# Optimization experiments

Measured on AMD Instinct MI355X. Metric: run time of the kernel, lower is better.

Reference implementation:

```python
import jax, jax.numpy as jnp
import numpy as np

N, E, B, EP = 100000, 1600000, 512, 200000
NIN, NEMB, HID, NL = 64, 64, 72, 3
EPS = 1e-5


def setup_inputs() -> dict:
    key = jax.random.key(0)
    ks = jax.random.split(key, 20)
    inp = {
        'x': jax.random.normal(ks[0], (N, NIN), jnp.float32),
        'emb': jax.random.normal(ks[1], (N, NEMB), jnp.float32),
        'assign': jax.random.uniform(ks[2], (N, B), jnp.float32),
        'edge_index': jax.random.randint(ks[3], (2, E), 0, N, jnp.int64),
        'pedge_index': jax.random.randint(ks[4], (2, EP), 0, B, jnp.int64),
        # params (xavier-ish scale)
        'node_w': jax.random.normal(ks[5], (NIN, HID), jnp.float32) / np.sqrt(NIN),
        'node_b': jnp.zeros((HID,), jnp.float32),
        'emb_w': jax.random.normal(ks[6], (NEMB, HID), jnp.float32) / np.sqrt(NEMB),
        'emb_b': jnp.zeros((HID,), jnp.float32),
        'conv_winit': jax.random.normal(ks[7], (NL, HID, HID), jnp.float32) / np.sqrt(HID),
        'conv_wroot': jax.random.normal(ks[8], (NL, HID, HID), jnp.float32) / np.sqrt(HID),
        'conv_bias': jnp.zeros((NL, HID), jnp.float32),
        'bn_gamma': jnp.ones((NL, HID), jnp.float32),
        'bn_beta': jnp.zeros((NL, HID), jnp.float32),
        'mlp_w1': jax.random.normal(ks[9], (12 * HID, HID), jnp.float32) / np.sqrt(12 * HID),
        'mlp_b1': jnp.zeros((HID,), jnp.float32),
        'mlp_w2': jax.random.normal(ks[10], (HID, 1), jnp.float32) / np.sqrt(HID),
        'mlp_b2': jnp.zeros((1,), jnp.float32),
    }
    return inp


def _forward(x, emb, assign, node_w, node_b, emb_w, emb_b, conv_winit,
             conv_wroot, conv_bias, bn_gamma, bn_beta, mlp_w1, mlp_b1,
             mlp_w2, mlp_b2, edge_index, pedge_index):
    n = x.shape[0]
    nb = assign.shape[1]
    row, col = edge_index[0], edge_index[1]
    # gcn_norm without self-loops (ARMAConv): D^{-1/2} A D^{-1/2}
    deg = jax.ops.segment_sum(jnp.ones((row.shape[0],), x.dtype), col, num_segments=n)
    dis = jnp.where(deg > 0, jax.lax.rsqrt(jnp.maximum(deg, 1.0)) * jnp.where(deg > 0, 1.0, 0.0), 0.0)
    dis = jnp.where(deg > 0, deg ** -0.5, 0.0)
    norm = dis[row] * dis[col]

    h = jax.nn.relu(x @ node_w + node_b)  # [N, HID]
    for l in range(NL):
        # ARMAConv K=1, T=1: relu(A_hat (h Wi) + h Wr + b)
        m = norm[:, None] * (h @ conv_winit[l])[row]        # [E, HID]
        agg = jax.ops.segment_sum(m, col, num_segments=n)   # [N, HID]
        h = jax.nn.relu(agg + h @ conv_wroot[l] + conv_bias[l])
        # F.relu applied again in forward (idempotent), then BatchNorm (training stats)
        mu = h.mean(0)
        var = ((h - mu) ** 2).mean(0)
        h = (h - mu) * jax.lax.rsqrt(var + EPS) * bn_gamma[l] + bn_beta[l]

    e = jax.nn.relu(emb @ emb_w + emb_b)
    z = jnp.concatenate([h, e], axis=-1)  # [N, 2*HID]

    batch = jnp.argmax(assign, axis=-1)
    cnt = jax.ops.segment_sum(jnp.ones((n,), z.dtype), batch, num_segments=nb)
    p1 = jax.ops.segment_sum(z, batch, num_segments=nb)
    p2 = jax.ops.segment_max(z, batch, num_segments=nb)
    p3 = p1 / jnp.maximum(cnt, 1.0)[:, None]
    xp = jnp.concatenate([p1, p2, p3], axis=-1)  # [B, 6*HID]

    pair = jnp.concatenate([xp[pedge_index[0]], xp[pedge_index[1]]], axis=1)  # [EP, 12*HID]
    out = jnp.tanh(pair @ mlp_w1 + mlp_b1) @ mlp_w2 + mlp_b2
    return out


def reference(x, emb, assign, edge_index, pedge_index, node_w, node_b, emb_w,
              emb_b, conv_winit, conv_wroot, conv_bias, bn_gamma, bn_beta,
              mlp_w1, mlp_b1, mlp_w2, mlp_b2):
    return _forward(x, emb, assign, node_w, node_b, emb_w, emb_b, conv_winit,
                    conv_wroot, conv_bias, bn_gamma, bn_beta, mlp_w1, mlp_b1,
                    mlp_w2, mlp_b2, edge_index, pedge_index)
```

## Files before the change

### kernel.cpp

```cpp
#include <hip/hip_runtime.h>
#include <hip/hip_bf16.h>

#define HID 72
#define EPSV 1e-5f
#define CAP 64
#define DP 76
#define NSH 32
#define GF 256
#define GA 2048

__device__ __forceinline__ float tanh_fast(float x) {
    float cx = fminf(fmaxf(x, -15.f), 15.f);
    float e = __expf(2.f * cx);
    return __fdividef(e - 1.f, e + 1.f);
}
__device__ __forceinline__ void fma4(float4& a, float w, const float4 v) {
    a.x += w * v.x; a.y += w * v.y; a.z += w * v.z; a.w += w * v.w;
}
__device__ __forceinline__ void add4(float4& a, const float4 v) {
    a.x += v.x; a.y += v.y; a.z += v.z; a.w += v.w;
}
__device__ __forceinline__ float inv_sqrt_deg(int d) {
    return (d > 0) ? rsqrtf((float)d) : 0.f;
}

__global__ __launch_bounds__(256) void k_d1(const float* __restrict__ x, const float* __restrict__ node_w,
                                            const float* __restrict__ node_b,
                                            const float* __restrict__ emb, const float* __restrict__ emb_w,
                                            const float* __restrict__ emb_b,
                                            float* __restrict__ t_buf, float* __restrict__ e_buf,
                                            int* __restrict__ deg, float* __restrict__ shadows,
                                            int* __restrict__ bcnt, int N, int B, int GD) {
    __shared__ float ws[HID][DP];
    int tid = threadIdx.x;
    int bid = blockIdx.x;
    if (bid >= 2 * GD) {
        int j = (bid - 2 * GD) * 256 + tid;
        if (j < N) deg[j] = 0;
        if (j < 3 * NSH * 2 * HID) shadows[j] = 0.f;
        if (j < B) bcnt[j] = 0;
        return;
    }
    const float* xin; const float* W; const float* bias; float* out;
    if (bid < GD) { xin = x;   W = node_w; bias = node_b; out = t_buf; }
    else          { xin = emb; W = emb_w;  bias = emb_b;  out = e_buf; bid -= GD; }
    int n0 = bid * 128;
    for (int i = tid; i < 64 * HID; i += 256) {
        int k = i / HID, f = i % HID;
        ws[f][k] = W[i];
    }
    __syncthreads();
    int tn = tid & 31;
    int tf = (tid >> 5) * 9;
    float acc[4][9];
    #pragma unroll
    for (int j = 0; j < 9; j++) {
        float b = bias[tf + j];
        acc[0][j] = b; acc[1][j] = b; acc[2][j] = b; acc[3][j] = b;
    }
    int g0 = n0 + tn;
    const float4* xp0 = (const float4*)(xin + (size_t)(g0      < N ? g0      : N - 1) * 64);
    const float4* xp1 = (const float4*)(xin + (size_t)(g0 + 32 < N ? g0 + 32 : N - 1) * 64);
    const float4* xp2 = (const float4*)(xin + (size_t)(g0 + 64 < N ? g0 + 64 : N - 1) * 64);
    const float4* xp3 = (const float4*)(xin + (size_t)(g0 + 96 < N ? g0 + 96 : N - 1) * 64);
    #pragma unroll 2
    for (int k4 = 0; k4 < 16; k4++) {
        float4 h0 = xp0[k4];
        float4 h1 = xp1[k4];
        float4 h2 = xp2[k4];
        float4 h3 = xp3[k4];
        int k = k4 * 4;
        #pragma unroll
        for (int j = 0; j < 9; j++) {
            float4 w = *(const float4*)&ws[tf + j][k];
            acc[0][j] += h0.x * w.x + h0.y * w.y + h0.z * w.z + h0.w * w.w;
            acc[1][j] += h1.x * w.x + h1.y * w.y + h1.z * w.z + h1.w * w.w;
            acc[2][j] += h2.x * w.x + h2.y * w.y + h2.z * w.z + h2.w * w.w;
            acc[3][j] += h3.x * w.x + h3.y * w.y + h3.z * w.z + h3.w * w.w;
        }
    }
    #pragma unroll
    for (int i = 0; i < 4; i++) {
        int gn = n0 + tn + 32 * i;
        if (gn >= N) continue;
        float* dst = out + (size_t)gn * HID + tf;
        #pragma unroll
        for (int j = 0; j < 9; j++) dst[j] = fmaxf(acc[i][j], 0.f);
    }
}

__global__ __launch_bounds__(256) void k_front2(const int* __restrict__ row, const int* __restrict__ col,
                                                int* __restrict__ deg, int* __restrict__ csr_r, int E,
                                                const float* __restrict__ t_buf,
                                                const float* __restrict__ wi0, const float* __restrict__ wr0,
                                                const float* __restrict__ cb0,
                                                float* __restrict__ hw, float* __restrict__ t2,
                                                const float* __restrict__ assign, int* __restrict__ batchv,
                                                int* __restrict__ bcnt, int N, int B, int GC) {
    __shared__ float ws[HID][DP];
    int tid = threadIdx.x;
    int bid = blockIdx.x;

    if (bid < GF) {
        int stride = GF * 256 * 8;
        for (int base = (bid * 256 + tid) * 8; base < E; base += stride) {
            #pragma unroll
            for (int h = 0; h < 2; h++) {
                int eb = base + h * 4;
                if (eb + 3 < E) {
                    int4 cc = *(const int4*)(col + eb);
                    int4 rr = *(const int4*)(row + eb);
                    int p0 = atomicAdd(&deg[cc.x], 1);
                    int p1 = atomicAdd(&deg[cc.y], 1);
                    int p2 = atomicAdd(&deg[cc.z], 1);
                    int p3 = atomicAdd(&deg[cc.w], 1);
                    if (p0 < CAP) csr_r[(size_t)cc.x * CAP + p0] = rr.x;
                    if (p1 < CAP) csr_r[(size_t)cc.y * CAP + p1] = rr.y;
                    if (p2 < CAP) csr_r[(size_t)cc.z * CAP + p2] = rr.z;
                    if (p3 < CAP) csr_r[(size_t)cc.w * CAP + p3] = rr.w;
                } else if (eb < E) {
                    int lim = (eb + 4 < E) ? eb + 4 : E;
                    for (int e = eb; e < lim; e++) {
                        int c = col[e];
                        int pos = atomicAdd(&deg[c], 1);
                        if (pos < CAP) csr_r[(size_t)c * CAP + pos] = row[e];
                    }
                }
            }
        }
        return;
    }
    bid -= GF;
    if (bid < 2 * GC) {
        const float* W; const float* bias; float* out;
        if (bid < GC) { W = wi0; bias = nullptr; out = hw; }
        else          { W = wr0; bias = cb0;     out = t2; bid -= GC; }
        int n0 = bid * 128;
        for (int i = tid; i < HID * HID; i += 256) {
            int k = i / HID, f = i % HID;
            ws[f][k] = W[i];
        }
        __syncthreads();
        int tn = tid & 31;
        int tf = (tid >> 5) * 9;
        float acc[4][9];
        #pragma unroll
        for (int j = 0; j < 9; j++) {
            float b = bias ? bias[tf + j] : 0.f;
            acc[0][j] = b; acc[1][j] = b; acc[2][j] = b; acc[3][j] = b;
        }
        int g0 = n0 + tn;
        const float* r0 = t_buf + (size_t)(g0      < N ? g0      : N - 1) * HID;
        const float* r1 = t_buf + (size_t)(g0 + 32 < N ? g0 + 32 : N - 1) * HID;
        const float* r2 = t_buf + (size_t)(g0 + 64 < N ? g0 + 64 : N - 1) * HID;
        const float* r3 = t_buf + (size_t)(g0 + 96 < N ? g0 + 96 : N - 1) * HID;
        #pragma unroll 2
        for (int k4 = 0; k4 < HID / 4; k4++) {
            int k = k4 * 4;
            float4 h0 = *(const float4*)(r0 + k);
            float4 h1 = *(const float4*)(r1 + k);
            float4 h2 = *(const float4*)(r2 + k);
            float4 h3 = *(const float4*)(r3 + k);
            #pragma unroll
            for (int j = 0; j < 9; j++) {
                float4 w = *(const float4*)&ws[tf + j][k];
                acc[0][j] += h0.x * w.x + h0.y * w.y + h0.z * w.z + h0.w * w.w;
                acc[1][j] += h1.x * w.x + h1.y * w.y + h1.z * w.z + h1.w * w.w;
                acc[2][j] += h2.x * w.x + h2.y * w.y + h2.z * w.z + h2.w * w.w;
                acc[3][j] += h3.x * w.x + h3.y * w.y + h3.z * w.z + h3.w * w.w;
            }
        }
        #pragma unroll
        for (int i = 0; i < 4; i++) {
            int gn = n0 + tn + 32 * i;
            if (gn >= N) continue;
            float* dst = out + (size_t)gn * HID + tf;
            #pragma unroll
            for (int j = 0; j < 9; j++) dst[j] = acc[i][j];
        }
        return;
    }
    bid -= 2 * GC;
    int wib = tid >> 6;
    int lane = tid & 63;
    int nq = B / 4;
    for (int n = bid * 4 + wib; n < N; n += GA * 4) {
        const float4* rp4 = (const float4*)(assign + (size_t)n * B);
        float best = -INFINITY;
        int bidx = 0x7fffffff;
        for (int q = lane; q < nq; q += 64) {
            float4 v = rp4[q];
            int j = q * 4;
            if (v.x > best) { best = v.x; bidx = j; }
            if (v.y > best) { best = v.y; bidx = j + 1; }
            if (v.z > best) { best = v.z; bidx = j + 2; }
            if (v.w > best) { best = v.w; bidx = j + 3; }
        }
        #pragma unroll
        for (int off = 32; off > 0; off >>= 1) {
            float ov = __shfl_down(best, off);
            int oi = __shfl_down(bidx, off);
            if (ov > best || (ov == best && oi < bidx)) { best = ov; bidx = oi; }
        }
        if (lane == 0) {
            batchv[n] = bidx;
            atomicAdd(&bcnt[bidx], 1);
        }
    }
}

template <int SCALED>
__global__ __launch_bounds__(256) void k_gather9(const float* __restrict__ hw, const int* __restrict__ deg,
                                                 const int* __restrict__ csr_r, const float* __restrict__ t2,
                                                 float* __restrict__ t, int N, float* __restrict__ shadow,
                                                 int scanB, const int* __restrict__ bcnt,
                                                 int* __restrict__ boffs, int* __restrict__ bcur) {
    if (scanB && blockIdx.x == gridDim.x - 1) {
        int lane = threadIdx.x;
        if (lane < 64) {
            int c[8];
            int tot = 0;
            int base = lane * 8;
            #pragma unroll
            for (int j = 0; j < 8; j++) {
                int idx = base + j;
                c[j] = (idx < scanB) ? bcnt[idx] : 0;
                tot += c[j];
            }
            int v = tot;
            #pragma unroll
            for (int off = 1; off < 64; off <<= 1) {
                int u = __shfl_up(v, off);
                if (lane >= off) v += u;
            }
            int run = v - tot;
            #pragma unroll
            for (int j = 0; j < 8; j++) {
                int idx = base + j;
                if (idx < scanB) {
                    boffs[idx] = run;
                    bcur[idx] = run;
                    run += c[j];
                }
            }
        }
        return;
    }
    __shared__ float s1[HID], s2[HID];
    int tx = threadIdx.x;
    if (tx < HID) { s1[tx] = 0.f; s2[tx] = 0.f; }
    __syncthreads();
    int tid = blockIdx.x * blockDim.x + tx;
    int n = tid / 9;
    int s = tid - n * 9;
    if (n < N) {
        const float4* t2row = (const float4*)(t2 + (size_t)n * HID) + s * 2;
        float4 a0 = t2row[0], a1 = t2row[1];
        float4 b0 = make_float4(0.f, 0.f, 0.f, 0.f), b1 = b0;
        int dn = deg[n];
        int d = (dn > CAP) ? CAP : dn;
        float disc = inv_sqrt_deg(dn);
        const int* crow = csr_r + (size_t)n * CAP;
        const float4* hb = (const float4*)hw + s * 2;
        for (int j0 = 0; j0 < d; j0 += 4) {
            int4 rr = *(const int4*)(crow + j0);
            int rem = d - j0;
            {
                const float4* hp = hb + (size_t)rr.x * 18;
                if (SCALED) { add4(b0, hp[0]); add4(b1, hp[1]); }
                else { float w = inv_sqrt_deg(deg[rr.x]); fma4(b0, w, hp[0]); fma4(b1, w, hp[1]); }
            }
            if (rem > 1) {
                const float4* hp = hb + (size_t)rr.y * 18;
                if (SCALED) { add4(b0, hp[0]); add4(b1, hp[1]); }
                else { float w = inv_sqrt_deg(deg[rr.y]); fma4(b0, w, hp[0]); fma4(b1, w, hp[1]); }
            }
            if (rem > 2) {
                const float4* hp = hb + (size_t)rr.z * 18;
                if (SCALED) { add4(b0, hp[0]); add4(b1, hp[1]); }
                else { float w = inv_sqrt_deg(deg[rr.z]); fma4(b0, w, hp[0]); fma4(b1, w, hp[1]); }
            }
            if (rem > 3) {
                const float4* hp = hb + (size_t)rr.w * 18;
                if (SCALED) { add4(b0, hp[0]); add4(b1, hp[1]); }
                else { float w = inv_sqrt_deg(deg[rr.w]); fma4(b0, w, hp[0]); fma4(b1, w, hp[1]); }
            }
        }
        fma4(a0, disc, b0);
        fma4(a1, disc, b1);
        a0 = make_float4(fmaxf(a0.x, 0.f), fmaxf(a0.y, 0.f), fmaxf(a0.z, 0.f), fmaxf(a0.w, 0.f));
        a1 = make_float4(fmaxf(a1.x, 0.f), fmaxf(a1.y, 0.f), fmaxf(a1.z, 0.f), fmaxf(a1.w, 0.f));
        float4* trow = (float4*)(t + (size_t)n * HID) + s * 2;
        trow[0] = a0;
        trow[1] = a1;
        int f0 = s * 8;
        atomicAdd(&s1[f0 + 0], a0.x); atomicAdd(&s2[f0 + 0], a0.x * a0.x);
        atomicAdd(&s1[f0 + 1], a0.y); atomicAdd(&s2[f0 + 1], a0.y * a0.y);
        atomicAdd(&s1[f0 + 2], a0.z); atomicAdd(&s2[f0 + 2], a0.z * a0.z);
        atomicAdd(&s1[f0 + 3], a0.w); atomicAdd(&s2[f0 + 3], a0.w * a0.w);
        atomicAdd(&s1[f0 + 4], a1.x); atomicAdd(&s2[f0 + 4], a1.x * a1.x);
        atomicAdd(&s1[f0 + 5], a1.y); atomicAdd(&s2[f0 + 5], a1.y * a1.y);
        atomicAdd(&s1[f0 + 6], a1.z); atomicAdd(&s2[f0 + 6], a1.z * a1.z);
        atomicAdd(&s1[f0 + 7], a1.w); atomicAdd(&s2[f0 + 7], a1.w * a1.w);
    }
    __syncthreads();
    if (tx < HID) {
        float* shrow = shadow + (size_t)(blockIdx.x & (NSH - 1)) * (2 * HID);
        atomicAdd(&shrow[tx], s1[tx]);
        atomicAdd(&shrow[HID + tx], s2[tx]);
    }
}

#define CP 76
__global__ __launch_bounds__(256) void k_conv_t(const float* __restrict__ t, const float* __restrict__ shadow,
                                                const float* __restrict__ gamma, const float* __restrict__ beta,
                                                const float* __restrict__ wi, const float* __restrict__ wr,
                                                const float* __restrict__ cb, float* __restrict__ hw,
                                                float* __restrict__ t2, const int* __restrict__ deg,
                                                int N, float invN, int gcBlocks,
                                                const int* __restrict__ batchv, int* __restrict__ bcur,
                                                int* __restrict__ nlist) {
    __shared__ float hs[64][CP];
    __shared__ float ws[2 * HID][CP];
    __shared__ float bns[2 * HID];
    int tid = threadIdx.x;
    if ((int)blockIdx.x >= gcBlocks) {
        int n = ((int)blockIdx.x - gcBlocks) * 256 + tid;
        if (n < N) {
            int b = batchv[n];
            int pos = atomicAdd(&bcur[b], 1);
            nlist[pos] = n;
        }
        return;
    }
    if (tid < 2 * HID) {
        float ssum = 0.f;
        #pragma unroll
        for (int c = 0; c < NSH; c++) ssum += shadow[c * 2 * HID + tid];
        bns[tid] = ssum;
    }
    for (int i = tid; i < HID * 2 * HID; i += 256) {
        int k = i / (2 * HID), f = i % (2 * HID);
        ws[f][k] = (f < HID) ? wi[k * HID + f] : wr[k * HID + (f - HID)];
    }
    __syncthreads();
    int n0 = blockIdx.x * 64;
    for (int i = tid; i < 64 * HID; i += 256) {
        int n = i / HID, f = i % HID;
        int gn = n0 + n;
        float v = (gn < N) ? t[(size_t)gn * HID + f] : 0.f;
        float mu = bns[f] * invN;
        float var = bns[HID + f] * invN - mu * mu;
        v = (v - mu) * rsqrtf(var + EPSV) * gamma[f] + beta[f];
        hs[n][f] = v;
    }
    __syncthreads();
    int tn = tid & 15;
    int tf = (tid >> 4) * 9;
    float acc[4][9];
    #pragma unroll
    for (int j = 0; j < 9; j++) {
        float b = (tf >= HID) ? cb[tf - HID + j] : 0.f;
        acc[0][j] = b; acc[1][j] = b; acc[2][j] = b; acc[3][j] = b;
    }
    #pragma unroll 2
    for (int k4 = 0; k4 < HID / 4; k4++) {
        int k = k4 * 4;
        float4 h0 = *(const float4*)&hs[tn][k];
        float4 h1 = *(const float4*)&hs[tn + 16][k];
        float4 h2 = *(const float4*)&hs[tn + 32][k];
        float4 h3 = *(const float4*)&hs[tn + 48][k];
        #pragma unroll
        for (int j = 0; j < 9; j++) {
            float4 w = *(const float4*)&ws[tf + j][k];
            acc[0][j] += h0.x * w.x + h0.y * w.y + h0.z * w.z + h0.w * w.w;
            acc[1][j] += h1.x * w.x + h1.y * w.y + h1.z * w.z + h1.w * w.w;
            acc[2][j] += h2.x * w.x + h2.y * w.y + h2.z * w.z + h2.w * w.w;
            acc[3][j] += h3.x * w.x + h3.y * w.y + h3.z * w.z + h3.w * w.w;
        }
    }
    #pragma unroll
    for (int i = 0; i < 4; i++) {
        int gn = n0 + tn + 16 * i;
        if (gn >= N) continue;
        if (tf < HID) {
            float dsc = inv_sqrt_deg(deg[gn]);
            float* dst = hw + (size_t)gn * HID + tf;
            #pragma unroll
            for (int j = 0; j < 9; j++) dst[j] = acc[i][j] * dsc;
        } else {
            float* dst = t2 + (size_t)gn * HID + (tf - HID);
            #pragma unroll
            for (int j = 0; j < 9; j++) dst[j] = acc[i][j];
        }
    }
}

__global__ __launch_bounds__(576) void k_poolB(const float* __restrict__ t2, const float* __restrict__ ebuf,
                                               const float* __restrict__ shadow2, const float* __restrict__ g2,
                                               const float* __restrict__ bt2, const int* __restrict__ boffs,
                                               const int* __restrict__ bcnt, const int* __restrict__ nlist,
                                               float* __restrict__ xp, float invN) {
    __shared__ float ls[4][2 * HID], lm[4][2 * HID];
    int b = blockIdx.x;
    int tid = threadIdx.x;
    int f = tid % (2 * HID);
    int ch = tid / (2 * HID);
    bool isH = f < HID;
    float a = 1.f, sh = 0.f;
    const float* src;
    if (isH) {
        float s1v = 0.f, s2v = 0.f;
        #pragma unroll
        for (int c = 0; c < NSH; c++) {
            s1v += shadow2[c * 2 * HID + f];
            s2v += shadow2[c * 2 * HID + HID + f];
        }
        float mu = s1v * invN;
        float var = s2v * invN - mu * mu;
        float inv = rsqrtf(var + EPSV);
        a = inv * g2[f];
        sh = bt2[f] - mu * a;
        src = t2 + f;
    } else {
        src = ebuf + (f - HID);
    }
    int s = boffs[b];
    int c = bcnt[b];
    int e = s + c;
    float sum = 0.f, mx = -INFINITY;
    for (int i = s + ch; i < e; i += 4) {
        float v = src[(size_t)nlist[i] * HID] * a + sh;
        sum += v;
        mx = fmaxf(mx, v);
    }
    ls[ch][f] = sum;
    lm[ch][f] = mx;
    __syncthreads();
    if (ch == 0) {
        float stot = ls[0][f] + ls[1][f] + ls[2][f] + ls[3][f];
        float mtot = fmaxf(fmaxf(lm[0][f], lm[1][f]), fmaxf(lm[2][f], lm[3][f]));
        float* xr = xp + (size_t)b * (6 * HID);
        xr[f] = stot;
        xr[2 * HID + f] = mtot;
        xr[4 * HID + f] = stot / fmaxf((float)c, 1.f);
    }
}

__global__ __launch_bounds__(192) void k_uv(const float* __restrict__ xp, const float* __restrict__ w1,
                                            const float* __restrict__ b1, float* __restrict__ U,
                                            float* __restrict__ V) {
    int b = blockIdx.x;
    int t = threadIdx.x;
    if (t >= 2 * HID) return;
    int half = t / HID;
    int f = t % HID;
    const float* xr = xp + (size_t)b * (6 * HID);
    const float* wb = w1 + (size_t)half * (6 * HID) * HID + f;
    float acc = (half == 0) ? b1[f] : 0.f;
    #pragma unroll 4
    for (int k = 0; k < 6 * HID; k++) acc += xr[k] * wb[(size_t)k * HID];
    if (half == 0) U[(size_t)b * HID + f] = acc;
    else           V[(size_t)b * HID + f] = acc;
}

__global__ __launch_bounds__(256) void k_edge(const int* __restrict__ pe, const float* __restrict__ U,
                                              const float* __restrict__ V, const float* __restrict__ w2,
                                              const float* __restrict__ b2, float* __restrict__ out, int EP) {
    int ep = blockIdx.x * blockDim.x + threadIdx.x;
    if (ep >= EP) return;
    int a = pe[ep];
    int b = pe[EP + ep];
    const float4* up = (const float4*)(U + (size_t)a * HID);
    const float4* vp = (const float4*)(V + (size_t)b * HID);
    float s = 0.f;
    #pragma unroll
    for (int q = 0; q < HID / 4; q++) {
        float4 u = up[q];
        float4 v = vp[q];
        s += tanh_fast(u.x + v.x) * w2[q * 4 + 0];
        s += tanh_fast(u.y + v.y) * w2[q * 4 + 1];
        s += tanh_fast(u.z + v.z) * w2[q * 4 + 2];
        s += tanh_fast(u.w + v.w) * w2[q * 4 + 3];
    }
    out[ep] = s + b2[0];
}

extern "C" void kernel_launch(void* const* d_in, const int* in_sizes, int n_in,
                              void* d_out, int out_size, void* d_ws, size_t ws_size,
                              hipStream_t stream) {
    const float* x       = (const float*)d_in[0];
    const float* emb     = (const float*)d_in[1];
    const float* assign  = (const float*)d_in[2];
    const int*   ei      = (const int*)d_in[3];
    const int*   pe      = (const int*)d_in[4];
    const float* node_w  = (const float*)d_in[5];
    const float* node_b  = (const float*)d_in[6];
    const float* emb_w   = (const float*)d_in[7];
    const float* emb_b   = (const float*)d_in[8];
    const float* conv_wi = (const float*)d_in[9];
    const float* conv_wr = (const float*)d_in[10];
    const float* conv_b  = (const float*)d_in[11];
    const float* bn_g    = (const float*)d_in[12];
    const float* bn_b    = (const float*)d_in[13];
    const float* w1      = (const float*)d_in[14];
    const float* b1      = (const float*)d_in[15];
    const float* w2      = (const float*)d_in[16];
    const float* b2      = (const float*)d_in[17];

    int N = in_sizes[0] / 64;
    int B = in_sizes[2] / N;
    int E = in_sizes[3] / 2;
    int EP = in_sizes[4] / 2;
    float invN = 1.0f / (float)N;

    char* wp = (char*)d_ws;
    auto alloc = [&](size_t nbytes) -> void* {
        void* p = (void*)wp;
        wp += (nbytes + 255) & ~(size_t)255;
        return p;
    };
    float* t_buf  = (float*)alloc((size_t)N * HID * 4);
    float* t2     = (float*)alloc((size_t)N * HID * 4);
    float* hw     = (float*)alloc((size_t)N * HID * 4);
    float* e_buf  = (float*)alloc((size_t)N * HID * 4);
    int*   csr_r  = (int*)alloc((size_t)N * CAP * 4);
    int*   deg    = (int*)alloc((size_t)N * 4);
    int*   batchv = (int*)alloc((size_t)N * 4);
    int*   nlist  = (int*)alloc((size_t)N * 4);
    float* shadows= (float*)alloc((size_t)3 * NSH * 2 * HID * 4);
    int*   bcnt   = (int*)alloc((size_t)B * 4);
    int*   boffs  = (int*)alloc((size_t)B * 4);
    int*   bcur   = (int*)alloc((size_t)B * 4);
    float* xp     = (float*)alloc((size_t)B * 6 * HID * 4);
    float* Ub     = (float*)alloc((size_t)B * HID * 4);
    float* Vb     = (float*)alloc((size_t)B * HID * 4);

    const int* row = ei;
    const int* col = ei + E;

    int GD   = (N + 127) / 128;
    int GC64 = (N + 63) / 64;
    int GZ   = (N + 255) / 256;
    int GG   = (9 * N + 255) / 256;
    size_t shl = (size_t)NSH * 2 * HID;

    k_d1<<<2 * GD + GZ, 256, 0, stream>>>(x, node_w, node_b, emb, emb_w, emb_b,
                                          t_buf, e_buf, deg, shadows, bcnt, N, B, GD);

    k_front2<<<GF + 2 * GD + GA, 256, 0, stream>>>(row, col, deg, csr_r, E,
                                                   t_buf, conv_wi, conv_wr, conv_b, hw, t2,
                                                   assign, batchv, bcnt, N, B, GD);

    k_gather9<0><<<GG + 1, 256, 0, stream>>>(hw, deg, csr_r, t2, t_buf, N, shadows,
                                             B, bcnt, boffs, bcur);

    k_conv_t<<<GC64 + GZ, 256, 0, stream>>>(t_buf, shadows, bn_g, bn_b,
                                            conv_wi + (size_t)HID * HID, conv_wr + (size_t)HID * HID,
                                            conv_b + HID, hw, t2, deg, N, invN, GC64,
                                            batchv, bcur, nlist);
    k_gather9<1><<<GG, 256, 0, stream>>>(hw, deg, csr_r, t2, t_buf, N, shadows + shl,
                                         0, nullptr, nullptr, nullptr);

    k_conv_t<<<GC64, 256, 0, stream>>>(t_buf, shadows + shl, bn_g + HID, bn_b + HID,
                                       conv_wi + (size_t)2 * HID * HID, conv_wr + (size_t)2 * HID * HID,
                                       conv_b + 2 * HID, hw, t2, deg, N, invN, GC64,
                                       nullptr, nullptr, nullptr);
    k_gather9<1><<<GG, 256, 0, stream>>>(hw, deg, csr_r, t2, t_buf, N, shadows + 2 * shl,
                                         0, nullptr, nullptr, nullptr);

    k_poolB<<<B, 576, 0, stream>>>(t_buf, e_buf, shadows + 2 * shl,
                                   bn_g + 2 * HID, bn_b + 2 * HID,
                                   boffs, bcnt, nlist, xp, invN);
    k_uv<<<B, 192, 0, stream>>>(xp, w1, b1, Ub, Vb);
    k_edge<<<(EP + 255) / 256, 256, 0, stream>>>(pe, Ub, Vb, w2, b2, (float*)d_out, EP);
}
```

Measured before the change: 1.316 ms.

## Split gather into 18 lanes per node, separate BN stats kernel, split conv by weight

```diff
diff --git a/kernel.cpp b/kernel.cpp
--- a/kernel.cpp
+++ b/kernel.cpp
@@ -5,7 +5,6 @@
 #define EPSV 1e-5f
 #define CAP 64
 #define DP 76
-#define NSH 32
 #define GF 256
 #define GA 2048
 
@@ -29,7 +28,7 @@
                                             const float* __restrict__ emb, const float* __restrict__ emb_w,
                                             const float* __restrict__ emb_b,
                                             float* __restrict__ t_buf, float* __restrict__ e_buf,
-                                            int* __restrict__ deg, float* __restrict__ shadows,
+                                            int* __restrict__ deg, float* __restrict__ stats,
                                             int* __restrict__ bcnt, int N, int B, int GD) {
     __shared__ float ws[HID][DP];
     int tid = threadIdx.x;
@@ -37,7 +36,7 @@
     if (bid >= 2 * GD) {
         int j = (bid - 2 * GD) * 256 + tid;
         if (j < N) deg[j] = 0;
-        if (j < 3 * NSH * 2 * HID) shadows[j] = 0.f;
+        if (j < 3 * 2 * HID) stats[j] = 0.f;
         if (j < B) bcnt[j] = 0;
         return;
     }
@@ -210,11 +209,11 @@
 }
 
 template <int SCALED>
-__global__ __launch_bounds__(256) void k_gather9(const float* __restrict__ hw, const int* __restrict__ deg,
-                                                 const int* __restrict__ csr_r, const float* __restrict__ t2,
-                                                 float* __restrict__ t, int N, float* __restrict__ shadow,
-                                                 int scanB, const int* __restrict__ bcnt,
-                                                 int* __restrict__ boffs, int* __restrict__ bcur) {
+__global__ __launch_bounds__(256) void k_gather18(const float* __restrict__ hw, const int* __restrict__ deg,
+                                                  const int* __restrict__ csr_r, const float* __restrict__ t2,
+                                                  float* __restrict__ t, int N,
+                                                  int scanB, const int* __restrict__ bcnt,
+                                                  int* __restrict__ boffs, int* __restrict__ bcur) {
     if (scanB && blockIdx.x == gridDim.x - 1) {
         int lane = threadIdx.x;
         if (lane < 64) {
@@ -246,86 +245,86 @@
         }
         return;
     }
+    int tid = blockIdx.x * blockDim.x + threadIdx.x;
+    int n = tid / 18;
+    int s = tid - n * 18;
+    if (n >= N) return;
+    float4 a0 = *((const float4*)(t2 + (size_t)n * HID) + s);
+    float4 b0 = make_float4(0.f, 0.f, 0.f, 0.f);
+    int dn = deg[n];
+    int d = (dn > CAP) ? CAP : dn;
+    float disc = inv_sqrt_deg(dn);
+    const int* crow = csr_r + (size_t)n * CAP;
+    const float4* hb = (const float4*)hw + s;
+    for (int j0 = 0; j0 < d; j0 += 4) {
+        int4 rr = *(const int4*)(crow + j0);
+        int rem = d - j0;
+        {
+            float4 hv = hb[(size_t)rr.x * 18];
+            if (SCALED) add4(b0, hv); else fma4(b0, inv_sqrt_deg(deg[rr.x]), hv);
+        }
+        if (rem > 1) {
+            float4 hv = hb[(size_t)rr.y * 18];
+            if (SCALED) add4(b0, hv); else fma4(b0, inv_sqrt_deg(deg[rr.y]), hv);
+        }
+        if (rem > 2) {
+            float4 hv = hb[(size_t)rr.z * 18];
+            if (SCALED) add4(b0, hv); else fma4(b0, inv_sqrt_deg(deg[rr.z]), hv);
+        }
+        if (rem > 3) {
+            float4 hv = hb[(size_t)rr.w * 18];
+            if (SCALED) add4(b0, hv); else fma4(b0, inv_sqrt_deg(deg[rr.w]), hv);
+        }
+    }
+    fma4(a0, disc, b0);
+    *((float4*)(t + (size_t)n * HID) + s) =
+        make_float4(fmaxf(a0.x, 0.f), fmaxf(a0.y, 0.f), fmaxf(a0.z, 0.f), fmaxf(a0.w, 0.f));
+}
+
+__global__ __launch_bounds__(256) void k_stats(const float* __restrict__ t, float* __restrict__ st, int total4) {
     __shared__ float s1[HID], s2[HID];
     int tx = threadIdx.x;
-    if (tx < HID) { s1[tx] = 0.f; s2[tx] = 0.f; }
+    if (tx < HID) s1[tx] = 0.f;
+    else if (tx < 2 * HID) s2[tx - HID] = 0.f;
     __syncthreads();
-    int tid = blockIdx.x * blockDim.x + tx;
-    int n = tid / 9;
-    int s = tid - n * 9;
-    if (n < N) {
-        const float4* t2row = (const float4*)(t2 + (size_t)n * HID) + s * 2;
-        float4 a0 = t2row[0], a1 = t2row[1];
-        float4 b0 = make_float4(0.f, 0.f, 0.f, 0.f), b1 = b0;
-        int dn = deg[n];
-        int d = (dn > CAP) ? CAP : dn;
-        float disc = inv_sqrt_deg(dn);
-        const int* crow = csr_r + (size_t)n * CAP;
-        const float4* hb = (const float4*)hw + s * 2;
-        for (int j0 = 0; j0 < d; j0 += 4) {
-            int4 rr = *(const int4*)(crow + j0);
-            int rem = d - j0;
-            {
-                const float4* hp = hb + (size_t)rr.x * 18;
-                if (SCALED) { add4(b0, hp[0]); add4(b1, hp[1]); }
-                else { float w = inv_sqrt_deg(deg[rr.x]); fma4(b0, w, hp[0]); fma4(b1, w, hp[1]); }
-            }
-            if (rem > 1) {
-                const float4* hp = hb + (size_t)rr.y * 18;
-                if (SCALED) { add4(b0, hp[0]); add4(b1, hp[1]); }
-                else { float w = inv_sqrt_deg(deg[rr.y]); fma4(b0, w, hp[0]); fma4(b1, w, hp[1]); }
-            }
-            if (rem > 2) {
-                const float4* hp = hb + (size_t)rr.z * 18;
-                if (SCALED) { add4(b0, hp[0]); add4(b1, hp[1]); }
-                else { float w = inv_sqrt_deg(deg[rr.z]); fma4(b0, w, hp[0]); fma4(b1, w, hp[1]); }
-            }
-            if (rem > 3) {
-                const float4* hp = hb + (size_t)rr.w * 18;
-                if (SCALED) { add4(b0, hp[0]); add4(b1, hp[1]); }
-                else { float w = inv_sqrt_deg(deg[rr.w]); fma4(b0, w, hp[0]); fma4(b1, w, hp[1]); }
-            }
-        }
-        fma4(a0, disc, b0);
-        fma4(a1, disc, b1);
-        a0 = make_float4(fmaxf(a0.x, 0.f), fmaxf(a0.y, 0.f), fmaxf(a0.z, 0.f), fmaxf(a0.w, 0.f));
-        a1 = make_float4(fmaxf(a1.x, 0.f), fmaxf(a1.y, 0.f), fmaxf(a1.z, 0.f), fmaxf(a1.w, 0.f));
-        float4* trow = (float4*)(t + (size_t)n * HID) + s * 2;
-        trow[0] = a0;
-        trow[1] = a1;
-        int f0 = s * 8;
-        atomicAdd(&s1[f0 + 0], a0.x); atomicAdd(&s2[f0 + 0], a0.x * a0.x);
-        atomicAdd(&s1[f0 + 1], a0.y); atomicAdd(&s2[f0 + 1], a0.y * a0.y);
-        atomicAdd(&s1[f0 + 2], a0.z); atomicAdd(&s2[f0 + 2], a0.z * a0.z);
-        atomicAdd(&s1[f0 + 3], a0.w); atomicAdd(&s2[f0 + 3], a0.w * a0.w);
-        atomicAdd(&s1[f0 + 4], a1.x); atomicAdd(&s2[f0 + 4], a1.x * a1.x);
-        atomicAdd(&s1[f0 + 5], a1.y); atomicAdd(&s2[f0 + 5], a1.y * a1.y);
-        atomicAdd(&s1[f0 + 6], a1.z); atomicAdd(&s2[f0 + 6], a1.z * a1.z);
-        atomicAdd(&s1[f0 + 7], a1.w); atomicAdd(&s2[f0 + 7], a1.w * a1.w);
-    }
+    int stride = gridDim.x * blockDim.x;
+    int i0 = blockIdx.x * blockDim.x + tx;
+    int f0 = (i0 * 4) % HID;
+    float a0 = 0, a1 = 0, a2 = 0, a3 = 0, q0 = 0, q1 = 0, q2 = 0, q3 = 0;
+    const float4* tp = (const float4*)t;
+    for (int i = i0; i < total4; i += stride) {
+        float4 v = tp[i];
+        a0 += v.x; q0 += v.x * v.x;
+        a1 += v.y; q1 += v.y * v.y;
+        a2 += v.z; q2 += v.z * v.z;
+        a3 += v.w; q3 += v.w * v.w;
+    }
+    atomicAdd(&s1[f0 + 0], a0); atomicAdd(&s2[f0 + 0], q0);
+    atomicAdd(&s1[f0 + 1], a1); atomicAdd(&s2[f0 + 1], q1);
+    atomicAdd(&s1[f0 + 2], a2); atomicAdd(&s2[f0 + 2], q2);
+    atomicAdd(&s1[f0 + 3], a3); atomicAdd(&s2[f0 + 3], q3);
     __syncthreads();
     if (tx < HID) {
-        float* shrow = shadow + (size_t)(blockIdx.x & (NSH - 1)) * (2 * HID);
-        atomicAdd(&shrow[tx], s1[tx]);
-        atomicAdd(&shrow[HID + tx], s2[tx]);
-    }
-}
-
-#define CP 76
-__global__ __launch_bounds__(256) void k_conv_t(const float* __restrict__ t, const float* __restrict__ shadow,
+        atomicAdd(&st[tx], s1[tx]);
+        atomicAdd(&st[HID + tx], s2[tx]);
+    }
+}
+
+__global__ __launch_bounds__(256) void k_conv_s(const float* __restrict__ t, const float* __restrict__ stats,
                                                 const float* __restrict__ gamma, const float* __restrict__ beta,
                                                 const float* __restrict__ wi, const float* __restrict__ wr,
                                                 const float* __restrict__ cb, float* __restrict__ hw,
                                                 float* __restrict__ t2, const int* __restrict__ deg,
-                                                int N, float invN, int gcBlocks,
+                                                int N, float invN, int GD,
                                                 const int* __restrict__ batchv, int* __restrict__ bcur,
                                                 int* __restrict__ nlist) {
-    __shared__ float hs[64][CP];
-    __shared__ float ws[2 * HID][CP];
-    __shared__ float bns[2 * HID];
+    __shared__ float ws[HID][DP];
+    __shared__ __align__(16) float bna[HID];
+    __shared__ __align__(16) float bnsh[HID];
     int tid = threadIdx.x;
-    if ((int)blockIdx.x >= gcBlocks) {
-        int n = ((int)blockIdx.x - gcBlocks) * 256 + tid;
+    int bid = blockIdx.x;
+    if (bid >= 2 * GD) {
+        int n = (bid - 2 * GD) * 256 + tid;
         if (n < N) {
             int b = batchv[n];
             int pos = atomicAdd(&bcur[b], 1);
@@ -333,43 +332,48 @@
         }
         return;
     }
-    if (tid < 2 * HID) {
-        float ssum = 0.f;
-        #pragma unroll
-        for (int c = 0; c < NSH; c++) ssum += shadow[c * 2 * HID + tid];
-        bns[tid] = ssum;
-    }
-    for (int i = tid; i < HID * 2 * HID; i += 256) {
-        int k = i / (2 * HID), f = i % (2 * HID);
-        ws[f][k] = (f < HID) ? wi[k * HID + f] : wr[k * HID + (f - HID)];
+    const float* W; bool isWi;
+    if (bid < GD) { W = wi; isWi = true; }
+    else          { W = wr; isWi = false; bid -= GD; }
+    if (tid < HID) {
+        float mu = stats[tid] * invN;
+        float var = stats[HID + tid] * invN - mu * mu;
+        float a = rsqrtf(var + EPSV) * gamma[tid];
+        bna[tid] = a;
+        bnsh[tid] = beta[tid] - mu * a;
+    }
+    for (int i = tid; i < HID * HID; i += 256) {
+        int k = i / HID, f = i % HID;
+        ws[f][k] = W[i];
     }
     __syncthreads();
-    int n0 = blockIdx.x * 64;
-    for (int i = tid; i < 64 * HID; i += 256) {
-        int n = i / HID, f = i % HID;
-        int gn = n0 + n;
-        float v = (gn < N) ? t[(size_t)gn * HID + f] : 0.f;
-        float mu = bns[f] * invN;
-        float var = bns[HID + f] * invN - mu * mu;
-        v = (v - mu) * rsqrtf(var + EPSV) * gamma[f] + beta[f];
-        hs[n][f] = v;
-    }
-    __syncthreads();
-    int tn = tid & 15;
-    int tf = (tid >> 4) * 9;
+    int n0 = bid * 128;
+    int tn = tid & 31;
+    int tf = (tid >> 5) * 9;
     float acc[4][9];
     #pragma unroll
     for (int j = 0; j < 9; j++) {
-        float b = (tf >= HID) ? cb[tf - HID + j] : 0.f;
+        float b = isWi ? 0.f : cb[tf + j];
         acc[0][j] = b; acc[1][j] = b; acc[2][j] = b; acc[3][j] = b;
     }
+    int g0 = n0 + tn;
+    const float* r0 = t + (size_t)(g0      < N ? g0      : N - 1) * HID;
+    const float* r1 = t + (size_t)(g0 + 32 < N ? g0 + 32 : N - 1) * HID;
+    const float* r2 = t + (size_t)(g0 + 64 < N ? g0 + 64 : N - 1) * HID;
+    const float* r3 = t + (size_t)(g0 + 96 < N ? g0 + 96 : N - 1) * HID;
     #pragma unroll 2
     for (int k4 = 0; k4 < HID / 4; k4++) {
         int k = k4 * 4;
-        float4 h0 = *(const float4*)&hs[tn][k];
-        float4 h1 = *(const float4*)&hs[tn + 16][k];
-        float4 h2 = *(const float4*)&hs[tn + 32][k];
-        float4 h3 = *(const float4*)&hs[tn + 48][k];
+        float4 av = *(const float4*)&bna[k];
+        float4 sv = *(const float4*)&bnsh[k];
+        float4 h0 = *(const float4*)(r0 + k);
+        float4 h1 = *(const float4*)(r1 + k);
+        float4 h2 = *(const float4*)(r2 + k);
+        float4 h3 = *(const float4*)(r3 + k);
+        h0.x = h0.x * av.x + sv.x; h0.y = h0.y * av.y + sv.y; h0.z = h0.z * av.z + sv.z; h0.w = h0.w * av.w + sv.w;
+        h1.x = h1.x * av.x + sv.x; h1.y = h1.y * av.y + sv.y; h1.z = h1.z * av.z + sv.z; h1.w = h1.w * av.w + sv.w;
+        h2.x = h2.x * av.x + sv.x; h2.y = h2.y * av.y + sv.y; h2.z = h2.z * av.z + sv.z; h2.w = h2.w * av.w + sv.w;
+        h3.x = h3.x * av.x + sv.x; h3.y = h3.y * av.y + sv.y; h3.z = h3.z * av.z + sv.z; h3.w = h3.w * av.w + sv.w;
         #pragma unroll
         for (int j = 0; j < 9; j++) {
             float4 w = *(const float4*)&ws[tf + j][k];
@@ -381,15 +385,15 @@
     }
     #pragma unroll
     for (int i = 0; i < 4; i++) {
-        int gn = n0 + tn + 16 * i;
+        int gn = n0 + tn + 32 * i;
         if (gn >= N) continue;
-        if (tf < HID) {
+        if (isWi) {
             float dsc = inv_sqrt_deg(deg[gn]);
             float* dst = hw + (size_t)gn * HID + tf;
             #pragma unroll
             for (int j = 0; j < 9; j++) dst[j] = acc[i][j] * dsc;
         } else {
-            float* dst = t2 + (size_t)gn * HID + (tf - HID);
+            float* dst = t2 + (size_t)gn * HID + tf;
             #pragma unroll
             for (int j = 0; j < 9; j++) dst[j] = acc[i][j];
         }
@@ -397,7 +401,7 @@
 }
 
 __global__ __launch_bounds__(576) void k_poolB(const float* __restrict__ t2, const float* __restrict__ ebuf,
-                                               const float* __restrict__ shadow2, const float* __restrict__ g2,
+                                               const float* __restrict__ stats2, const float* __restrict__ g2,
                                                const float* __restrict__ bt2, const int* __restrict__ boffs,
                                                const int* __restrict__ bcnt, const int* __restrict__ nlist,
                                                float* __restrict__ xp, float invN) {
@@ -410,12 +414,7 @@
     float a = 1.f, sh = 0.f;
     const float* src;
     if (isH) {
-        float s1v = 0.f, s2v = 0.f;
-        #pragma unroll
-        for (int c = 0; c < NSH; c++) {
-            s1v += shadow2[c * 2 * HID + f];
-            s2v += shadow2[c * 2 * HID + HID + f];
-        }
+        float s1v = stats2[f], s2v = stats2[HID + f];
         float mu = s1v * invN;
         float var = s2v * invN - mu * mu;
         float inv = rsqrtf(var + EPSV);
@@ -528,7 +527,7 @@
     int*   deg    = (int*)alloc((size_t)N * 4);
     int*   batchv = (int*)alloc((size_t)N * 4);
     int*   nlist  = (int*)alloc((size_t)N * 4);
-    float* shadows= (float*)alloc((size_t)3 * NSH * 2 * HID * 4);
+    float* stats  = (float*)alloc((size_t)3 * 2 * HID * 4);
     int*   bcnt   = (int*)alloc((size_t)B * 4);
     int*   boffs  = (int*)alloc((size_t)B * 4);
     int*   bcur   = (int*)alloc((size_t)B * 4);
@@ -540,36 +539,37 @@
     const int* col = ei + E;
 
     int GD   = (N + 127) / 128;
-    int GC64 = (N + 63) / 64;
     int GZ   = (N + 255) / 256;
-    int GG   = (9 * N + 255) / 256;
-    size_t shl = (size_t)NSH * 2 * HID;
+    int GG18 = (18 * N + 255) / 256;
 
     k_d1<<<2 * GD + GZ, 256, 0, stream>>>(x, node_w, node_b, emb, emb_w, emb_b,
-                                          t_buf, e_buf, deg, shadows, bcnt, N, B, GD);
+                                          t_buf, e_buf, deg, stats, bcnt, N, B, GD);
 
     k_front2<<<GF + 2 * GD + GA, 256, 0, stream>>>(row, col, deg, csr_r, E,
                                                    t_buf, conv_wi, conv_wr, conv_b, hw, t2,
                                                    assign, batchv, bcnt, N, B, GD);
 
-    k_gather9<0><<<GG + 1, 256, 0, stream>>>(hw, deg, csr_r, t2, t_buf, N, shadows,
-                                             B, bcnt, boffs, bcur);
-
-    k_conv_t<<<GC64 + GZ, 256, 0, stream>>>(t_buf, shadows, bn_g, bn_b,
-                                            conv_wi + (size_t)HID * HID, conv_wr + (size_t)HID * HID,
-                                            conv_b + HID, hw, t2, deg, N, invN, GC64,
-                                            batchv, bcur, nlist);
-    k_gather9<1><<<GG, 256, 0, stream>>>(hw, deg, csr_r, t2, t_buf, N, shadows + shl,
-                                         0, nullptr, nullptr, nullptr);
-
-    k_conv_t<<<GC64, 256, 0, stream>>>(t_buf, shadows + shl, bn_g + HID, bn_b + HID,
-                                       conv_wi + (size_t)2 * HID * HID, conv_wr + (size_t)2 * HID * HID,
-                                       conv_b + 2 * HID, hw, t2, deg, N, invN, GC64,
-                                       nullptr, nullptr, nullptr);
-    k_gather9<1><<<GG, 256, 0, stream>>>(hw, deg, csr_r, t2, t_buf, N, shadows + 2 * shl,
-                                         0, nullptr, nullptr, nullptr);
-
-    k_poolB<<<B, 576, 0, stream>>>(t_buf, e_buf, shadows + 2 * shl,
+    k_gather18<0><<<GG18 + 1, 256, 0, stream>>>(hw, deg, csr_r, t2, t_buf, N,
+                                                B, bcnt, boffs, bcur);
+    k_stats<<<288, 256, 0, stream>>>(t_buf, stats, N * HID / 4);
+
+    k_conv_s<<<2 * GD + GZ, 256, 0, stream>>>(t_buf, stats, bn_g, bn_b,
+                                              conv_wi + (size_t)HID * HID, conv_wr + (size_t)HID * HID,
+                                              conv_b + HID, hw, t2, deg, N, invN, GD,
+                                              batchv, bcur, nlist);
+    k_gather18<1><<<GG18, 256, 0, stream>>>(hw, deg, csr_r, t2, t_buf, N,
+                                            0, nullptr, nullptr, nullptr);
+    k_stats<<<288, 256, 0, stream>>>(t_buf, stats + 2 * HID, N * HID / 4);
+
+    k_conv_s<<<2 * GD, 256, 0, stream>>>(t_buf, stats + 2 * HID, bn_g + HID, bn_b + HID,
+                                         conv_wi + (size_t)2 * HID * HID, conv_wr + (size_t)2 * HID * HID,
+                                         conv_b + 2 * HID, hw, t2, deg, N, invN, GD,
+                                         nullptr, nullptr, nullptr);
+    k_gather18<1><<<GG18, 256, 0, stream>>>(hw, deg, csr_r, t2, t_buf, N,
+                                            0, nullptr, nullptr, nullptr);
+    k_stats<<<288, 256, 0, stream>>>(t_buf, stats + 4 * HID, N * HID / 4);
+
+    k_poolB<<<B, 576, 0, stream>>>(t_buf, e_buf, stats + 4 * HID,
                                    bn_g + 2 * HID, bn_b + 2 * HID,
                                    boffs, bcnt, nlist, xp, invN);
     k_uv<<<B, 192, 0, stream>>>(xp, w1, b1, Ub, Vb);
```

Measured after the change: 1.177 ms. 1.12x faster.
